# Kernel tuning notes

Measured on AMD Instinct MI355X. Metric: run time of the kernel, lower is better.

## Reference

```python
import jax, jax.numpy as jnp
import numpy as np

B, C, L = 8192, 1, 4096
SCALES = 5
OUT_DIM = 512
STD_FACTOR = 1.0
SQRT_HALF = 0.7071067811865476  # Haar filter coefficient 1/sqrt(2)


def setup_inputs() -> dict:
    key = jax.random.key(0)
    k1, k2 = jax.random.split(key)
    x = jax.random.normal(k1, (B, C, L), dtype=jnp.float32)
    # kaiming_uniform_(a=0): bound = sqrt(2) * sqrt(3 / fan_in)
    fan_in = L  # in_dim_wave == in_dim for dyadic Haar
    bound = np.sqrt(2.0) * np.sqrt(3.0 / fan_in)
    block_mat = jax.random.uniform(k2, (L, OUT_DIM), dtype=jnp.float32,
                                   minval=-bound, maxval=bound)
    return {"x": x, "block_mat": block_mat}


def haar_analysis(x, scales):
    """Multi-level Haar DWT over last axis. Returns [cA_n, cD_n, ..., cD_1]."""
    details = []
    cur = x
    for _ in range(scales):
        even, odd = cur[..., ::2], cur[..., 1::2]
        details.append((even - odd) * SQRT_HALF)  # highpass
        cur = (even + odd) * SQRT_HALF            # lowpass
    return [cur] + details[::-1]


def reference(x, block_mat):
    coeffs = haar_analysis(x, SCALES)
    x_freq_cat = jnp.concatenate(coeffs, axis=-1)        # [B, C, L]
    c_no = x_freq_cat.shape[-1]
    x_freq_mat = x_freq_cat.reshape(-1, c_no)            # [B*C, L]
    a = jnp.abs(x_freq_mat)
    # torch.std is unbiased (ddof=1)
    threshold = jnp.mean(a) + jnp.std(a, ddof=1) * STD_FACTOR
    mask = a > threshold
    # sparse.mm(sparse(masked x), W) == (x * mask) @ W
    x_sparse = jnp.where(mask, x_freq_mat, jnp.zeros((), x_freq_mat.dtype))
    out = jax.nn.relu(x_sparse @ block_mat)              # [B*C, OUT_DIM]
    return out.reshape(x_freq_cat.shape[:-1] + (OUT_DIM,))
```

## Files before the change

kernel.cpp:

```cpp
#include <hip/hip_runtime.h>
#include <hip/hip_bf16.h>
#include <math.h>

#define LDIM 4096
#define NROWS 8192
#define NOUT 512

static const float SQRT_HALF_F = 0.70710678118654752440f;

typedef __attribute__((ext_vector_type(8))) short short8;
typedef __attribute__((ext_vector_type(4))) float f32x4;

#define AM_OFF   0ull
#define WT_OFF   67108864ull
#define PART_OFF (WT_OFF + 4194304ull)
#define THR_OFF  (PART_OFF + 131072ull)

__device__ inline unsigned short f2bf(float f) {
  union { float f; unsigned u; } v; v.f = f;
  unsigned r = (v.u + 0x7fffu + ((v.u >> 16) & 1u)) >> 16;
  return (unsigned short)r;
}

__device__ inline void async16(void* l, const void* g) {
  __builtin_amdgcn_global_load_lds((const __attribute__((address_space(1))) void*)g,
                                   (__attribute__((address_space(3))) void*)l, 16, 0, 0);
}

__global__ __launch_bounds__(256) void haar1_kernel(const float* __restrict__ x,
                                                    double* __restrict__ partials) {
  __shared__ __align__(16) float bufA[4096];
  __shared__ __align__(16) float bufB[2048];
  __shared__ double red[8];

  const int row = blockIdx.x;
  const int tid = threadIdx.x;
  const float S = SQRT_HALF_F;

  const float4* xr = (const float4*)(x + (size_t)row * LDIM);
  float4* bA4 = (float4*)bufA;
#pragma unroll
  for (int k = 0; k < 4; ++k) bA4[tid + k * 256] = xr[tid + k * 256];
  __syncthreads();

  double sa = 0.0, sq = 0.0;

#pragma unroll
  for (int k = 0; k < 8; ++k) {
    int i = tid + k * 256;
    float e = bufA[2 * i], o = bufA[2 * i + 1];
    float d = (e - o) * S, ap = (e + o) * S;
    sa += (double)fabsf(d); sq += (double)d * (double)d;
    bufB[i] = ap;
  }
  __syncthreads();
#pragma unroll
  for (int k = 0; k < 4; ++k) {
    int i = tid + k * 256;
    float e = bufB[2 * i], o = bufB[2 * i + 1];
    float d = (e - o) * S, ap = (e + o) * S;
    sa += (double)fabsf(d); sq += (double)d * (double)d;
    bufA[i] = ap;
  }
  __syncthreads();
#pragma unroll
  for (int k = 0; k < 2; ++k) {
    int i = tid + k * 256;
    float e = bufA[2 * i], o = bufA[2 * i + 1];
    float d = (e - o) * S, ap = (e + o) * S;
    sa += (double)fabsf(d); sq += (double)d * (double)d;
    bufB[i] = ap;
  }
  __syncthreads();
  {
    int i = tid;
    float e = bufB[2 * i], o = bufB[2 * i + 1];
    float d = (e - o) * S, ap = (e + o) * S;
    sa += (double)fabsf(d); sq += (double)d * (double)d;
    bufA[i] = ap;
  }
  __syncthreads();
  if (tid < 128) {
    int i = tid;
    float e = bufA[2 * i], o = bufA[2 * i + 1];
    float d = (e - o) * S, ap = (e + o) * S;
    sa += (double)fabsf(d) + (double)fabsf(ap);
    sq += (double)d * (double)d + (double)ap * (double)ap;
  }

  const int lane = tid & 63, wid = tid >> 6;
#pragma unroll
  for (int off = 32; off > 0; off >>= 1) {
    sa += __shfl_down(sa, off, 64);
    sq += __shfl_down(sq, off, 64);
  }
  if (lane == 0) { red[wid] = sa; red[4 + wid] = sq; }
  __syncthreads();
  if (tid == 0) {
    partials[2 * (size_t)row + 0] = red[0] + red[1] + red[2] + red[3];
    partials[2 * (size_t)row + 1] = red[4] + red[5] + red[6] + red[7];
  }
}

__global__ __launch_bounds__(256) void thr_kernel(const double* __restrict__ partials,
                                                  float* __restrict__ thr) {
  __shared__ double red[8];
  const int tid = threadIdx.x;
  double sa = 0.0, sq = 0.0;
#pragma unroll
  for (int k = 0; k < NROWS / 256; ++k) {
    int i = tid + k * 256;
    sa += partials[2 * i + 0];
    sq += partials[2 * i + 1];
  }
  const int lane = tid & 63, wid = tid >> 6;
#pragma unroll
  for (int off = 32; off > 0; off >>= 1) {
    sa += __shfl_down(sa, off, 64);
    sq += __shfl_down(sq, off, 64);
  }
  if (lane == 0) { red[wid] = sa; red[4 + wid] = sq; }
  __syncthreads();
  if (tid == 0) {
    double s = red[0] + red[1] + red[2] + red[3];
    double q = red[4] + red[5] + red[6] + red[7];
    const double n = (double)NROWS * (double)LDIM;
    double mean = s / n;
    double var = (q - s * s / n) / (n - 1.0);
    *thr = (float)(mean + sqrt(var));
  }
}

__global__ __launch_bounds__(256) void haar2_kernel(const float* __restrict__ x,
                                                    const float* __restrict__ thrp,
                                                    unsigned short* __restrict__ Am) {
  __shared__ __align__(16) float bufA[4096];
  __shared__ __align__(16) float bufB[2048];
  __shared__ __align__(16) unsigned short rowD[4096];

  const float thr = *thrp;
  const int row = blockIdx.x;
  const int tid = threadIdx.x;
  const float S = SQRT_HALF_F;

  const float4* xr = (const float4*)(x + (size_t)row * LDIM);
  float4* bA4 = (float4*)bufA;
#pragma unroll
  for (int k = 0; k < 4; ++k) bA4[tid + k * 256] = xr[tid + k * 256];
  __syncthreads();

#pragma unroll
  for (int k = 0; k < 8; ++k) {
    int i = tid + k * 256;
    float e = bufA[2 * i], o = bufA[2 * i + 1];
    float d = (e - o) * S, ap = (e + o) * S;
    rowD[2048 + i] = f2bf((fabsf(d) > thr) ? d : 0.0f);
    bufB[i] = ap;
  }
  __syncthreads();
#pragma unroll
  for (int k = 0; k < 4; ++k) {
    int i = tid + k * 256;
    float e = bufB[2 * i], o = bufB[2 * i + 1];
    float d = (e - o) * S, ap = (e + o) * S;
    rowD[1024 + i] = f2bf((fabsf(d) > thr) ? d : 0.0f);
    bufA[i] = ap;
  }
  __syncthreads();
#pragma unroll
  for (int k = 0; k < 2; ++k) {
    int i = tid + k * 256;
    float e = bufA[2 * i], o = bufA[2 * i + 1];
    float d = (e - o) * S, ap = (e + o) * S;
    rowD[512 + i] = f2bf((fabsf(d) > thr) ? d : 0.0f);
    bufB[i] = ap;
  }
  __syncthreads();
  {
    int i = tid;
    float e = bufB[2 * i], o = bufB[2 * i + 1];
    float d = (e - o) * S, ap = (e + o) * S;
    rowD[256 + i] = f2bf((fabsf(d) > thr) ? d : 0.0f);
    bufA[i] = ap;
  }
  __syncthreads();
  if (tid < 128) {
    int i = tid;
    float e = bufA[2 * i], o = bufA[2 * i + 1];
    float d = (e - o) * S, ap = (e + o) * S;
    rowD[128 + i] = f2bf((fabsf(d) > thr) ? d : 0.0f);
    rowD[i] = f2bf((fabsf(ap) > thr) ? ap : 0.0f);
  }
  __syncthreads();

  short8* dst = (short8*)(Am + (size_t)row * LDIM);
  const short8* src = (const short8*)rowD;
  dst[tid] = src[tid];
  dst[tid + 256] = src[tid + 256];
}

__global__ __launch_bounds__(256) void wcvt_kernel(const float* __restrict__ W,
                                                   unsigned short* __restrict__ Wt) {
  __shared__ float tile[32][33];
  const int bx = blockIdx.x;
  const int by = blockIdx.y;
  const int tx = threadIdx.x & 31, ty = threadIdx.x >> 5;
#pragma unroll
  for (int j = 0; j < 4; ++j)
    tile[ty + j * 8][tx] = W[(size_t)(by * 32 + ty + j * 8) * NOUT + bx * 32 + tx];
  __syncthreads();
#pragma unroll
  for (int j = 0; j < 4; ++j)
    Wt[(size_t)(bx * 32 + ty + j * 8) * LDIM + by * 32 + tx] = f2bf(tile[tx][ty + j * 8]);
}

__global__ __launch_bounds__(256) void gemm_kernel(const unsigned short* __restrict__ Am,
                                                   const unsigned short* __restrict__ Wt,
                                                   float* __restrict__ out) {
  __shared__ __align__(16) unsigned short As[128 * 64];
  __shared__ __align__(16) unsigned short Bs[64 * 64];

  const int tid = threadIdx.x;
  const int lane = tid & 63, w = tid >> 6;
  const int quad = lane >> 4, l15 = lane & 15;

  const int id = blockIdx.x;
  const int xcd = id & 7, slot = id >> 3;
  const int nblk = slot & 7;
  const int mblk = (slot >> 3) * 8 + xcd;
  const int n0 = nblk * 64, m0 = mblk * 128;

  f32x4 acc[2][4] = {};

  const int rl = lane >> 3;
  const int cg = (lane & 7) ^ rl;
  const unsigned short* AgBase = Am + (size_t)(m0 + rl) * LDIM + cg * 8;
  const unsigned short* BgBase = Wt + (size_t)(n0 + rl) * LDIM + cg * 8;

  for (int k0 = 0; k0 < LDIM; k0 += 64) {
#pragma unroll
    for (int j = 0; j < 4; ++j)
      async16(&As[(w * 4 + j) * 512], AgBase + (size_t)((w * 4 + j) * 8) * LDIM + k0);
#pragma unroll
    for (int j = 0; j < 2; ++j)
      async16(&Bs[(w * 2 + j) * 512], BgBase + (size_t)((w * 2 + j) * 8) * LDIM + k0);
    __syncthreads();

    short8 af[2][2], bf[4][2];
#pragma unroll
    for (int mi = 0; mi < 2; ++mi) {
      const int row = w * 32 + mi * 16 + l15;
#pragma unroll
      for (int ks = 0; ks < 2; ++ks)
        af[mi][ks] = *(const short8*)&As[row * 64 + ((ks * 4 + quad) ^ (row & 7)) * 8];
    }
#pragma unroll
    for (int ni = 0; ni < 4; ++ni) {
      const int row = ni * 16 + l15;
#pragma unroll
      for (int ks = 0; ks < 2; ++ks)
        bf[ni][ks] = *(const short8*)&Bs[row * 64 + ((ks * 4 + quad) ^ (row & 7)) * 8];
    }
#pragma unroll
    for (int ks = 0; ks < 2; ++ks)
#pragma unroll
      for (int mi = 0; mi < 2; ++mi)
#pragma unroll
        for (int ni = 0; ni < 4; ++ni)
          acc[mi][ni] = __builtin_amdgcn_mfma_f32_16x16x32_bf16(af[mi][ks], bf[ni][ks],
                                                                acc[mi][ni], 0, 0, 0);
    __syncthreads();
  }

#pragma unroll
  for (int mi = 0; mi < 2; ++mi) {
#pragma unroll
    for (int ni = 0; ni < 4; ++ni) {
      const int r0 = m0 + w * 32 + mi * 16 + quad * 4;
      const int c = n0 + ni * 16 + l15;
#pragma unroll
      for (int r = 0; r < 4; ++r)
        out[(size_t)(r0 + r) * NOUT + c] = fmaxf(acc[mi][ni][r], 0.0f);
    }
  }
}

extern "C" void kernel_launch(void* const* d_in, const int* in_sizes, int n_in,
                              void* d_out, int out_size, void* d_ws, size_t ws_size,
                              hipStream_t stream) {
  const float* x = (const float*)d_in[0];
  const float* W = (const float*)d_in[1];
  float* out = (float*)d_out;

  char* ws = (char*)d_ws;
  unsigned short* Am = (unsigned short*)(ws + AM_OFF);
  unsigned short* Wt = (unsigned short*)(ws + WT_OFF);
  double* partials = (double*)(ws + PART_OFF);
  float* thr = (float*)(ws + THR_OFF);

  haar1_kernel<<<NROWS, 256, 0, stream>>>(x, partials);
  wcvt_kernel<<<dim3(NOUT / 32, LDIM / 32), 256, 0, stream>>>(W, Wt);
  thr_kernel<<<1, 256, 0, stream>>>(partials, thr);
  haar2_kernel<<<NROWS, 256, 0, stream>>>(x, thr, Am);
  gemm_kernel<<<512, 256, 0, stream>>>(Am, Wt, out);
}
```

Measured before the change: 275.5 us.

## Compute Haar levels in registers per thread instead of shared-memory passes

Both Haar kernels now give each thread 16 contiguous inputs, so four decomposition levels run entirely in registers, and a single lane shuffle handles the fifth level. This removes the LDS staging buffers and the series of __syncthreads barriers between levels. haar2 writes its masked bf16 coefficients straight to global memory as vector stores instead of assembling the row in LDS first. The cost is more registers per thread and smaller, less coalesced global stores for the coarse levels.

```diff
diff --git a/kernel.cpp b/kernel.cpp
--- a/kernel.cpp
+++ b/kernel.cpp
@@ -10,6 +10,9 @@
 
 typedef __attribute__((ext_vector_type(8))) short short8;
 typedef __attribute__((ext_vector_type(4))) float f32x4;
+typedef __attribute__((ext_vector_type(8))) unsigned short u16x8;
+typedef __attribute__((ext_vector_type(4))) unsigned short u16x4;
+typedef __attribute__((ext_vector_type(2))) unsigned short u16x2;
 
 #define AM_OFF   0ull
 #define WT_OFF   67108864ull
@@ -22,73 +25,66 @@
   return (unsigned short)r;
 }
 
+__device__ inline unsigned short mcvt(float f, float thr) {
+  return f2bf((fabsf(f) > thr) ? f : 0.0f);
+}
+
 __device__ inline void async16(void* l, const void* g) {
   __builtin_amdgcn_global_load_lds((const __attribute__((address_space(1))) void*)g,
                                    (__attribute__((address_space(3))) void*)l, 16, 0, 0);
 }
 
+
 __global__ __launch_bounds__(256) void haar1_kernel(const float* __restrict__ x,
                                                     double* __restrict__ partials) {
-  __shared__ __align__(16) float bufA[4096];
-  __shared__ __align__(16) float bufB[2048];
   __shared__ double red[8];
-
   const int row = blockIdx.x;
-  const int tid = threadIdx.x;
+  const int t = threadIdx.x;
   const float S = SQRT_HALF_F;
 
-  const float4* xr = (const float4*)(x + (size_t)row * LDIM);
-  float4* bA4 = (float4*)bufA;
-#pragma unroll
-  for (int k = 0; k < 4; ++k) bA4[tid + k * 256] = xr[tid + k * 256];
-  __syncthreads();
+  const float4* xr = (const float4*)(x + (size_t)row * LDIM) + 4 * t;
+  float v[16];
+#pragma unroll
+  for (int k = 0; k < 4; ++k) {
+    float4 q = xr[k];
+    v[4 * k] = q.x; v[4 * k + 1] = q.y; v[4 * k + 2] = q.z; v[4 * k + 3] = q.w;
+  }
 
   double sa = 0.0, sq = 0.0;
-
-#pragma unroll
-  for (int k = 0; k < 8; ++k) {
-    int i = tid + k * 256;
-    float e = bufA[2 * i], o = bufA[2 * i + 1];
-    float d = (e - o) * S, ap = (e + o) * S;
-    sa += (double)fabsf(d); sq += (double)d * (double)d;
-    bufB[i] = ap;
-  }
-  __syncthreads();
-#pragma unroll
-  for (int k = 0; k < 4; ++k) {
-    int i = tid + k * 256;
-    float e = bufB[2 * i], o = bufB[2 * i + 1];
-    float d = (e - o) * S, ap = (e + o) * S;
-    sa += (double)fabsf(d); sq += (double)d * (double)d;
-    bufA[i] = ap;
-  }
-  __syncthreads();
-#pragma unroll
-  for (int k = 0; k < 2; ++k) {
-    int i = tid + k * 256;
-    float e = bufA[2 * i], o = bufA[2 * i + 1];
-    float d = (e - o) * S, ap = (e + o) * S;
-    sa += (double)fabsf(d); sq += (double)d * (double)d;
-    bufB[i] = ap;
-  }
-  __syncthreads();
-  {
-    int i = tid;
-    float e = bufB[2 * i], o = bufB[2 * i + 1];
-    float d = (e - o) * S, ap = (e + o) * S;
-    sa += (double)fabsf(d); sq += (double)d * (double)d;
-    bufA[i] = ap;
-  }
-  __syncthreads();
-  if (tid < 128) {
-    int i = tid;
-    float e = bufA[2 * i], o = bufA[2 * i + 1];
-    float d = (e - o) * S, ap = (e + o) * S;
-    sa += (double)fabsf(d) + (double)fabsf(ap);
-    sq += (double)d * (double)d + (double)ap * (double)ap;
-  }
-
-  const int lane = tid & 63, wid = tid >> 6;
+  float a1[8], a2[4], a3[2], a4;
+#pragma unroll
+  for (int j = 0; j < 8; ++j) {
+    float d = (v[2 * j] - v[2 * j + 1]) * S;
+    a1[j] = (v[2 * j] + v[2 * j + 1]) * S;
+    sa += (double)fabsf(d); sq += (double)d * (double)d;
+  }
+#pragma unroll
+  for (int j = 0; j < 4; ++j) {
+    float d = (a1[2 * j] - a1[2 * j + 1]) * S;
+    a2[j] = (a1[2 * j] + a1[2 * j + 1]) * S;
+    sa += (double)fabsf(d); sq += (double)d * (double)d;
+  }
+#pragma unroll
+  for (int j = 0; j < 2; ++j) {
+    float d = (a2[2 * j] - a2[2 * j + 1]) * S;
+    a3[j] = (a2[2 * j] + a2[2 * j + 1]) * S;
+    sa += (double)fabsf(d); sq += (double)d * (double)d;
+  }
+  {
+    float d = (a3[0] - a3[1]) * S;
+    a4 = (a3[0] + a3[1]) * S;
+    sa += (double)fabsf(d); sq += (double)d * (double)d;
+  }
+  {
+    float other = __shfl_xor(a4, 1, 64);
+    if ((t & 1) == 0) {
+      float d = (a4 - other) * S, ap = (a4 + other) * S;
+      sa += (double)fabsf(d) + (double)fabsf(ap);
+      sq += (double)d * (double)d + (double)ap * (double)ap;
+    }
+  }
+
+  const int lane = t & 63, wid = t >> 6;
 #pragma unroll
   for (int off = 32; off > 0; off >>= 1) {
     sa += __shfl_down(sa, off, 64);
@@ -96,7 +92,7 @@
   }
   if (lane == 0) { red[wid] = sa; red[4 + wid] = sq; }
   __syncthreads();
-  if (tid == 0) {
+  if (t == 0) {
     partials[2 * (size_t)row + 0] = red[0] + red[1] + red[2] + red[3];
     partials[2 * (size_t)row + 1] = red[4] + red[5] + red[6] + red[7];
   }
@@ -134,69 +130,62 @@
 __global__ __launch_bounds__(256) void haar2_kernel(const float* __restrict__ x,
                                                     const float* __restrict__ thrp,
                                                     unsigned short* __restrict__ Am) {
-  __shared__ __align__(16) float bufA[4096];
-  __shared__ __align__(16) float bufB[2048];
-  __shared__ __align__(16) unsigned short rowD[4096];
-
   const float thr = *thrp;
   const int row = blockIdx.x;
-  const int tid = threadIdx.x;
+  const int t = threadIdx.x;
   const float S = SQRT_HALF_F;
 
-  const float4* xr = (const float4*)(x + (size_t)row * LDIM);
-  float4* bA4 = (float4*)bufA;
-#pragma unroll
-  for (int k = 0; k < 4; ++k) bA4[tid + k * 256] = xr[tid + k * 256];
-  __syncthreads();
-
-#pragma unroll
-  for (int k = 0; k < 8; ++k) {
-    int i = tid + k * 256;
-    float e = bufA[2 * i], o = bufA[2 * i + 1];
-    float d = (e - o) * S, ap = (e + o) * S;
-    rowD[2048 + i] = f2bf((fabsf(d) > thr) ? d : 0.0f);
-    bufB[i] = ap;
-  }
-  __syncthreads();
+  const float4* xr = (const float4*)(x + (size_t)row * LDIM) + 4 * t;
+  float v[16];
 #pragma unroll
   for (int k = 0; k < 4; ++k) {
-    int i = tid + k * 256;
-    float e = bufB[2 * i], o = bufB[2 * i + 1];
-    float d = (e - o) * S, ap = (e + o) * S;
-    rowD[1024 + i] = f2bf((fabsf(d) > thr) ? d : 0.0f);
-    bufA[i] = ap;
-  }
-  __syncthreads();
-#pragma unroll
-  for (int k = 0; k < 2; ++k) {
-    int i = tid + k * 256;
-    float e = bufA[2 * i], o = bufA[2 * i + 1];
-    float d = (e - o) * S, ap = (e + o) * S;
-    rowD[512 + i] = f2bf((fabsf(d) > thr) ? d : 0.0f);
-    bufB[i] = ap;
-  }
-  __syncthreads();
-  {
-    int i = tid;
-    float e = bufB[2 * i], o = bufB[2 * i + 1];
-    float d = (e - o) * S, ap = (e + o) * S;
-    rowD[256 + i] = f2bf((fabsf(d) > thr) ? d : 0.0f);
-    bufA[i] = ap;
-  }
-  __syncthreads();
-  if (tid < 128) {
-    int i = tid;
-    float e = bufA[2 * i], o = bufA[2 * i + 1];
-    float d = (e - o) * S, ap = (e + o) * S;
-    rowD[128 + i] = f2bf((fabsf(d) > thr) ? d : 0.0f);
-    rowD[i] = f2bf((fabsf(ap) > thr) ? ap : 0.0f);
-  }
-  __syncthreads();
-
-  short8* dst = (short8*)(Am + (size_t)row * LDIM);
-  const short8* src = (const short8*)rowD;
-  dst[tid] = src[tid];
-  dst[tid + 256] = src[tid + 256];
+    float4 q = xr[k];
+    v[4 * k] = q.x; v[4 * k + 1] = q.y; v[4 * k + 2] = q.z; v[4 * k + 3] = q.w;
+  }
+
+  unsigned short* orow = Am + (size_t)row * LDIM;
+  float a1[8], a2[4], a3[2], a4;
+
+  u16x8 d1;
+#pragma unroll
+  for (int j = 0; j < 8; ++j) {
+    float d = (v[2 * j] - v[2 * j + 1]) * S;
+    a1[j] = (v[2 * j] + v[2 * j + 1]) * S;
+    d1[j] = mcvt(d, thr);
+  }
+  *(u16x8*)(orow + 2048 + 8 * t) = d1;
+
+  u16x4 d2;
+#pragma unroll
+  for (int j = 0; j < 4; ++j) {
+    float d = (a1[2 * j] - a1[2 * j + 1]) * S;
+    a2[j] = (a1[2 * j] + a1[2 * j + 1]) * S;
+    d2[j] = mcvt(d, thr);
+  }
+  *(u16x4*)(orow + 1024 + 4 * t) = d2;
+
+  u16x2 d3;
+#pragma unroll
+  for (int j = 0; j < 2; ++j) {
+    float d = (a2[2 * j] - a2[2 * j + 1]) * S;
+    a3[j] = (a2[2 * j] + a2[2 * j + 1]) * S;
+    d3[j] = mcvt(d, thr);
+  }
+  *(u16x2*)(orow + 512 + 2 * t) = d3;
+
+  {
+    float d = (a3[0] - a3[1]) * S;
+    a4 = (a3[0] + a3[1]) * S;
+    orow[256 + t] = mcvt(d, thr);
+  }
+  {
+    float other = __shfl_xor(a4, 1, 64);
+    if ((t & 1) == 0) {
+      float d = (a4 - other) * S, ap = (a4 + other) * S;
+      orow[128 + t / 2] = mcvt(d, thr);
+      orow[t / 2] = mcvt(ap, thr);
+    }
+  }
 }
 
 __global__ __launch_bounds__(256) void wcvt_kernel(const float* __restrict__ W,
```

Measured after the change: 273.9 us. About the same (-0.6%).
